# Kernel tuning notes

Measured on AMD Instinct MI355X. Metric: run time of the kernel, lower is better.

## Reference

```python
import jax, jax.numpy as jnp
import numpy as np

N = 20000          # nodes
E = 640000         # edges (avg in-degree 32)
H = 8              # attention heads
CK = 32            # key/query channels per degree
CV = 32            # value channels per degree
DK = 16            # per-head key dim = (32*1 + 32*3)/8
KEY_FEATS = 128    # key_fiber.num_features = 32*1 + 32*3
DV = 4             # fused value degree dim = 1 + 3


def setup_inputs() -> dict:
    key = jax.random.key(0)
    k1, k2, k3, k4, k5 = jax.random.split(key, 5)
    return {
        "key": jax.random.normal(k1, (E, H, DK), dtype=jnp.float32),
        "query_0": jax.random.normal(k2, (N, CK, 1), dtype=jnp.float32),
        "query_1": jax.random.normal(k3, (N, CK, 3), dtype=jnp.float32),
        "value": jax.random.normal(k4, (E, CV, DV), dtype=jnp.float32),
        "edge_dst": jnp.sort(jax.random.randint(k5, (E,), 0, N, dtype=jnp.int32)),
    }


def reference(key, query_0, query_1, value, edge_dst):
    # fuse query degrees and split into heads: (N, C, 1+3) -> (N, H, DK)
    q = jnp.concatenate([query_0, query_1], axis=-1).reshape(N, H, DK)
    # e_dot_v: per-edge dot product with destination-node query -> (E, H)
    ew = jnp.einsum('ehd,ehd->eh', key, q[edge_dst]) / np.float32(np.sqrt(KEY_FEATS))
    # edge_softmax grouped by destination node (numerically stable)
    m = jax.ops.segment_max(ew, edge_dst, num_segments=N, indices_are_sorted=True)
    ex = jnp.exp(ew - m[edge_dst])
    den = jax.ops.segment_sum(ex, edge_dst, num_segments=N, indices_are_sorted=True)
    w = ex / den[edge_dst]                       # (E, H)
    # weighted sum of multi-degree values, scattered to destination nodes
    v = value.reshape(E, H, CV // H, DV)         # (E, H, C/H, DV)
    weighted = (w[:, :, None, None] * v).reshape(E, H * (CV // H) * DV)
    feat = jax.ops.segment_sum(weighted, edge_dst, num_segments=N,
                               indices_are_sorted=True).reshape(N, CV, DV)
    # unfuse_features: split last dim by degree dims (1, 3)
    return feat[..., :1], feat[..., 1:]
```

## Files before the change

### kernel.cpp

```cpp
#include <hip/hip_runtime.h>
#include <math.h>

#define NN 20000
#define EE 640000

__global__ __launch_bounds__(256)
void build_offsets(const int* __restrict__ dst, int* __restrict__ offs) {
    int e = blockIdx.x * 256 + threadIdx.x;
    if (e >= EE) return;
    int d = dst[e];
    if (e == 0) {
        for (int j = 0; j <= d; ++j) offs[j] = 0;
    } else {
        int dp = dst[e - 1];
        for (int j = dp + 1; j <= d; ++j) offs[j] = e;
    }
    if (e == EE - 1) {
        for (int j = d + 1; j <= NN; ++j) offs[j] = EE;
    }
}

__device__ __forceinline__ float4 ld4(const float* p) { return *(const float4*)p; }

__global__ __launch_bounds__(256)
void attn_se3_kernel(const float* __restrict__ key,
                     const float* __restrict__ q0,
                     const float* __restrict__ q1,
                     const float* __restrict__ val,
                     const int*   __restrict__ offs,
                     float*       __restrict__ out)
{
    const int wid  = threadIdx.x >> 6;
    const int lane = threadIdx.x & 63;
    const int n    = blockIdx.x * 4 + wid;
    const int s    = lane >> 5;
    const int cl   = lane & 31;

    float4 qv;
    qv.x = q0[n * 32 + cl];
    qv.y = q1[n * 96 + cl * 3 + 0];
    qv.z = q1[n * 96 + cl * 3 + 1];
    qv.w = q1[n * 96 + cl * 3 + 2];

    const int start = offs[n];
    const int end   = offs[n + 1];
    const int deg   = end - start;

    const float scale = 0.08838834764831845f;
    float  l   = 0.0f;
    float4 acc = make_float4(0.f, 0.f, 0.f, 0.f);

    const int co = cl * 4;
    int eA = start + s;
    float4 kA = make_float4(0,0,0,0), vA = kA, kB = kA, vB = kA;
    if (eA < end) {
        kA = ld4(key + (size_t)eA * 128 + co);
        vA = ld4(val + (size_t)eA * 128 + co);
    }
    if (eA + 2 < end) {
        kB = ld4(key + (size_t)(eA + 2) * 128 + co);
        vB = ld4(val + (size_t)(eA + 2) * 128 + co);
    }

    const int iters = (deg + 3) >> 2;
    for (int i = 0; i < iters; ++i) {
        const int eN = eA + 4;
        float4 kA2 = make_float4(0,0,0,0), vA2 = kA2, kB2 = kA2, vB2 = kA2;
        if (eN < end) {
            kA2 = ld4(key + (size_t)eN * 128 + co);
            vA2 = ld4(val + (size_t)eN * 128 + co);
        }
        if (eN + 2 < end) {
            kB2 = ld4(key + (size_t)(eN + 2) * 128 + co);
            vB2 = ld4(val + (size_t)(eN + 2) * 128 + co);
        }

        float pA = fmaf(kA.x, qv.x, fmaf(kA.y, qv.y, fmaf(kA.z, qv.z, kA.w * qv.w)));
        pA += __shfl_xor(pA, 1);
        pA += __shfl_xor(pA, 2);
        float pB = fmaf(kB.x, qv.x, fmaf(kB.y, qv.y, fmaf(kB.z, qv.z, kB.w * qv.w)));
        pB += __shfl_xor(pB, 1);
        pB += __shfl_xor(pB, 2);

        const float wA = (eA < end)     ? __expf(pA * scale) : 0.0f;
        const float wB = (eA + 2 < end) ? __expf(pB * scale) : 0.0f;

        l += wA + wB;
        acc.x = fmaf(wA, vA.x, acc.x);
        acc.y = fmaf(wA, vA.y, acc.y);
        acc.z = fmaf(wA, vA.z, acc.z);
        acc.w = fmaf(wA, vA.w, acc.w);
        acc.x = fmaf(wB, vB.x, acc.x);
        acc.y = fmaf(wB, vB.y, acc.y);
        acc.z = fmaf(wB, vB.z, acc.z);
        acc.w = fmaf(wB, vB.w, acc.w);

        kA = kA2; vA = vA2; kB = kB2; vB = vB2;
        eA = eN;
    }

    const float l2 = __shfl_xor(l, 32);
    float4 a2;
    a2.x = __shfl_xor(acc.x, 32);
    a2.y = __shfl_xor(acc.y, 32);
    a2.z = __shfl_xor(acc.z, 32);
    a2.w = __shfl_xor(acc.w, 32);
    const float ll = l + l2;

    if (lane < 32) {
        const float inv = (ll > 0.f) ? 1.0f / ll : 0.0f;
        out[n * 32 + cl] = (acc.x + a2.x) * inv;
        float* o1 = out + NN * 32 + n * 96 + cl * 3;
        o1[0] = (acc.y + a2.y) * inv;
        o1[1] = (acc.z + a2.z) * inv;
        o1[2] = (acc.w + a2.w) * inv;
    }
}

extern "C" void kernel_launch(void* const* d_in, const int* in_sizes, int n_in,
                              void* d_out, int out_size, void* d_ws, size_t ws_size,
                              hipStream_t stream) {
    const float* key = (const float*)d_in[0];
    const float* q0  = (const float*)d_in[1];
    const float* q1  = (const float*)d_in[2];
    const float* val = (const float*)d_in[3];
    const int*   dst = (const int*)d_in[4];
    float* out = (float*)d_out;
    int*   offs = (int*)d_ws;

    build_offsets<<<(EE + 255) / 256, 256, 0, stream>>>(dst, offs);
    attn_se3_kernel<<<NN / 4, 256, 0, stream>>>(key, q0, q1, val, offs, out);
}
```

Measured before the change: 629.1 us.

## Switch to edge-tiled parallelism with atomic segment accumulation and finalize pass

```diff
diff --git a/kernel.cpp b/kernel.cpp
--- a/kernel.cpp
+++ b/kernel.cpp
@@ -3,118 +3,116 @@
 
 #define NN 20000
 #define EE 640000
+#define TILE 32
+#define NWAVES (EE / TILE)
+#define STEPS (TILE / 2)
+
+#define OUT_F4 (NN * 32)
+#define L_F4   (NN * 2)
+#define Z_TOT  (OUT_F4 + L_F4)
 
 __global__ __launch_bounds__(256)
-void build_offsets(const int* __restrict__ dst, int* __restrict__ offs) {
-    int e = blockIdx.x * 256 + threadIdx.x;
-    if (e >= EE) return;
-    int d = dst[e];
-    if (e == 0) {
-        for (int j = 0; j <= d; ++j) offs[j] = 0;
-    } else {
-        int dp = dst[e - 1];
-        for (int j = dp + 1; j <= d; ++j) offs[j] = e;
-    }
-    if (e == EE - 1) {
-        for (int j = d + 1; j <= NN; ++j) offs[j] = EE;
-    }
+void zero_accum(float4* __restrict__ out4, float4* __restrict__ l4) {
+    int i = blockIdx.x * 256 + threadIdx.x;
+    float4 z = make_float4(0.f, 0.f, 0.f, 0.f);
+    if (i < OUT_F4) out4[i] = z;
+    else if (i < Z_TOT) l4[i - OUT_F4] = z;
 }
 
-__device__ __forceinline__ float4 ld4(const float* p) { return *(const float4*)p; }
+__global__ __launch_bounds__(256)
+void attn_edges(const float* __restrict__ key,
+                const float* __restrict__ q0,
+                const float* __restrict__ q1,
+                const float* __restrict__ val,
+                const int*   __restrict__ dst,
+                float*       __restrict__ out,
+                float*       __restrict__ lsum)
+{
+    const int wid  = blockIdx.x * 4 + (threadIdx.x >> 6);
+    const int lane = threadIdx.x & 63;
+    const int s    = lane >> 5;
+    const int cl   = lane & 31;
+    const int t    = wid * TILE;
+
+    const int dreg = dst[t + cl];
+
+    const float* kp = key + (size_t)(t + s) * 128 + cl * 4;
+    const float* vp = val + (size_t)(t + s) * 128 + cl * 4;
+    const float scale = 0.08838834764831845f;
+
+    int cur_n = __shfl(dreg, s);
+    float4 qv;
+    qv.x = q0[cur_n * 32 + cl];
+    qv.y = q1[cur_n * 96 + cl * 3 + 0];
+    qv.z = q1[cur_n * 96 + cl * 3 + 1];
+    qv.w = q1[cur_n * 96 + cl * 3 + 2];
+
+    float  lrun = 0.f;
+    float4 acc  = make_float4(0.f, 0.f, 0.f, 0.f);
+
+    float4 kb[3], vb[3];
+    kb[0] = *(const float4*)(kp);        vb[0] = *(const float4*)(vp);
+    kb[1] = *(const float4*)(kp + 256);  vb[1] = *(const float4*)(vp + 256);
+    kb[2] = *(const float4*)(kp + 512);  vb[2] = *(const float4*)(vp + 512);
+
+    #pragma unroll
+    for (int j = 0; j < STEPS; ++j) {
+        const float4 kc = kb[j % 3];
+        const float4 vc = vb[j % 3];
+        if (j + 3 < STEPS) {
+            kb[j % 3] = *(const float4*)(kp + (size_t)(j + 3) * 256);
+            vb[j % 3] = *(const float4*)(vp + (size_t)(j + 3) * 256);
+        }
+
+        const int n = __shfl(dreg, 2 * j + s);
+        if (n != cur_n) {
+            atomicAdd(&out[cur_n * 32 + cl], acc.x);
+            float* o1 = out + NN * 32 + cur_n * 96 + cl * 3;
+            atomicAdd(o1 + 0, acc.y);
+            atomicAdd(o1 + 1, acc.z);
+            atomicAdd(o1 + 2, acc.w);
+            if ((cl & 3) == 0) atomicAdd(&lsum[cur_n * 8 + (cl >> 2)], lrun);
+            acc  = make_float4(0.f, 0.f, 0.f, 0.f);
+            lrun = 0.f;
+            cur_n = n;
+            qv.x = q0[n * 32 + cl];
+            qv.y = q1[n * 96 + cl * 3 + 0];
+            qv.z = q1[n * 96 + cl * 3 + 1];
+            qv.w = q1[n * 96 + cl * 3 + 2];
+        }
+
+        float p = fmaf(kc.x, qv.x, fmaf(kc.y, qv.y, fmaf(kc.z, qv.z, kc.w * qv.w)));
+        p += __shfl_xor(p, 1);
+        p += __shfl_xor(p, 2);
+        const float w = __expf(p * scale);
+
+        lrun += w;
+        acc.x = fmaf(w, vc.x, acc.x);
+        acc.y = fmaf(w, vc.y, acc.y);
+        acc.z = fmaf(w, vc.z, acc.z);
+        acc.w = fmaf(w, vc.w, acc.w);
+    }
+
+    atomicAdd(&out[cur_n * 32 + cl], acc.x);
+    float* o1 = out + NN * 32 + cur_n * 96 + cl * 3;
+    atomicAdd(o1 + 0, acc.y);
+    atomicAdd(o1 + 1, acc.z);
+    atomicAdd(o1 + 2, acc.w);
+    if ((cl & 3) == 0) atomicAdd(&lsum[cur_n * 8 + (cl >> 2)], lrun);
+}
 
 __global__ __launch_bounds__(256)
-void attn_se3_kernel(const float* __restrict__ key,
-                     const float* __restrict__ q0,
-                     const float* __restrict__ q1,
-                     const float* __restrict__ val,
-                     const int*   __restrict__ offs,
-                     float*       __restrict__ out)
-{
-    const int wid  = threadIdx.x >> 6;
-    const int lane = threadIdx.x & 63;
-    const int n    = blockIdx.x * 4 + wid;
-    const int s    = lane >> 5;
-    const int cl   = lane & 31;
-
-    float4 qv;
-    qv.x = q0[n * 32 + cl];
-    qv.y = q1[n * 96 + cl * 3 + 0];
-    qv.z = q1[n * 96 + cl * 3 + 1];
-    qv.w = q1[n * 96 + cl * 3 + 2];
-
-    const int start = offs[n];
-    const int end   = offs[n + 1];
-    const int deg   = end - start;
-
-    const float scale = 0.08838834764831845f;
-    float  l   = 0.0f;
-    float4 acc = make_float4(0.f, 0.f, 0.f, 0.f);
-
-    const int co = cl * 4;
-    int eA = start + s;
-    float4 kA = make_float4(0,0,0,0), vA = kA, kB = kA, vB = kA;
-    if (eA < end) {
-        kA = ld4(key + (size_t)eA * 128 + co);
-        vA = ld4(val + (size_t)eA * 128 + co);
-    }
-    if (eA + 2 < end) {
-        kB = ld4(key + (size_t)(eA + 2) * 128 + co);
-        vB = ld4(val + (size_t)(eA + 2) * 128 + co);
-    }
-
-    const int iters = (deg + 3) >> 2;
-    for (int i = 0; i < iters; ++i) {
-        const int eN = eA + 4;
-        float4 kA2 = make_float4(0,0,0,0), vA2 = kA2, kB2 = kA2, vB2 = kA2;
-        if (eN < end) {
-            kA2 = ld4(key + (size_t)eN * 128 + co);
-            vA2 = ld4(val + (size_t)eN * 128 + co);
-        }
-        if (eN + 2 < end) {
-            kB2 = ld4(key + (size_t)(eN + 2) * 128 + co);
-            vB2 = ld4(val + (size_t)(eN + 2) * 128 + co);
-        }
-
-        float pA = fmaf(kA.x, qv.x, fmaf(kA.y, qv.y, fmaf(kA.z, qv.z, kA.w * qv.w)));
-        pA += __shfl_xor(pA, 1);
-        pA += __shfl_xor(pA, 2);
-        float pB = fmaf(kB.x, qv.x, fmaf(kB.y, qv.y, fmaf(kB.z, qv.z, kB.w * qv.w)));
-        pB += __shfl_xor(pB, 1);
-        pB += __shfl_xor(pB, 2);
-
-        const float wA = (eA < end)     ? __expf(pA * scale) : 0.0f;
-        const float wB = (eA + 2 < end) ? __expf(pB * scale) : 0.0f;
-
-        l += wA + wB;
-        acc.x = fmaf(wA, vA.x, acc.x);
-        acc.y = fmaf(wA, vA.y, acc.y);
-        acc.z = fmaf(wA, vA.z, acc.z);
-        acc.w = fmaf(wA, vA.w, acc.w);
-        acc.x = fmaf(wB, vB.x, acc.x);
-        acc.y = fmaf(wB, vB.y, acc.y);
-        acc.z = fmaf(wB, vB.z, acc.z);
-        acc.w = fmaf(wB, vB.w, acc.w);
-
-        kA = kA2; vA = vA2; kB = kB2; vB = vB2;
-        eA = eN;
-    }
-
-    const float l2 = __shfl_xor(l, 32);
-    float4 a2;
-    a2.x = __shfl_xor(acc.x, 32);
-    a2.y = __shfl_xor(acc.y, 32);
-    a2.z = __shfl_xor(acc.z, 32);
-    a2.w = __shfl_xor(acc.w, 32);
-    const float ll = l + l2;
-
-    if (lane < 32) {
-        const float inv = (ll > 0.f) ? 1.0f / ll : 0.0f;
-        out[n * 32 + cl] = (acc.x + a2.x) * inv;
-        float* o1 = out + NN * 32 + n * 96 + cl * 3;
-        o1[0] = (acc.y + a2.y) * inv;
-        o1[1] = (acc.z + a2.z) * inv;
-        o1[2] = (acc.w + a2.w) * inv;
-    }
+void finalize(float* __restrict__ out, const float* __restrict__ lsum) {
+    const int i = blockIdx.x * 256 + threadIdx.x;
+    const int n = i >> 5;
+    const int c = i & 31;
+    const float li = lsum[n * 8 + (c >> 2)];
+    const float inv = (li > 0.f) ? 1.0f / li : 0.0f;
+    out[i] *= inv;
+    float* o1 = out + NN * 32 + (size_t)n * 96 + c * 3;
+    o1[0] *= inv;
+    o1[1] *= inv;
+    o1[2] *= inv;
 }
 
 extern "C" void kernel_launch(void* const* d_in, const int* in_sizes, int n_in,
@@ -125,9 +123,10 @@
     const float* q1  = (const float*)d_in[2];
     const float* val = (const float*)d_in[3];
     const int*   dst = (const int*)d_in[4];
-    float* out = (float*)d_out;
-    int*   offs = (int*)d_ws;
+    float* out  = (float*)d_out;
+    float* lsum = (float*)d_ws;
 
-    build_offsets<<<(EE + 255) / 256, 256, 0, stream>>>(dst, offs);
-    attn_se3_kernel<<<NN / 4, 256, 0, stream>>>(key, q0, q1, val, offs, out);
+    zero_accum<<<(Z_TOT + 255) / 256, 256, 0, stream>>>((float4*)out, (float4*)lsum);
+    attn_edges<<<NWAVES / 4, 256, 0, stream>>>(key, q0, q1, val, dst, out, lsum);
+    finalize<<<(NN * 32) / 256, 256, 0, stream>>>(out, lsum);
 }
```

Result: slower. 664.1 us (+5.6%).
